# Kernel tuning notes

Measured on AMD Instinct MI355X. Metric: run time of the kernel, lower is better.

## Reference

```python
import jax, jax.numpy as jnp
import numpy as np

B, T, C, H = 4, 2048, 1024, 16
D = C // H
EPS = 1e-5


def setup_inputs() -> dict:
    key = jax.random.key(0)
    ks = jax.random.split(key, 8)
    s = 0.02
    return {
        "hidden_states": jax.random.normal(ks[0], (B, T, C), jnp.float32),
        "w_attn": jax.random.normal(ks[1], (C, 3 * C), jnp.float32) * s,
        "b_attn": jnp.zeros((3 * C,), jnp.float32),
        "w_proj": jax.random.normal(ks[2], (C, C), jnp.float32) * s,
        "b_proj": jnp.zeros((C,), jnp.float32),
        "ln1_g": jnp.ones((C,), jnp.float32),
        "ln1_b": jnp.zeros((C,), jnp.float32),
        "ln2_g": jnp.ones((C,), jnp.float32),
        "ln2_b": jnp.zeros((C,), jnp.float32),
        "w_fc": jax.random.normal(ks[3], (C, 4 * C), jnp.float32) * s,
        "b_fc": jnp.zeros((4 * C,), jnp.float32),
        "w_fc2": jax.random.normal(ks[4], (4 * C, C), jnp.float32) * s,
        "b_fc2": jnp.zeros((C,), jnp.float32),
    }


def _layernorm(x, g, b):
    mu = jnp.mean(x, axis=-1, keepdims=True)
    var = jnp.mean(jnp.square(x - mu), axis=-1, keepdims=True)
    return (x - mu) * jax.lax.rsqrt(var + EPS) * g + b


def _attention(x, w_attn, b_attn, w_proj, b_proj):
    Bx, Tx, Cx = x.shape
    qkv = x @ w_attn + b_attn  # [B,T,3C]  (GCLinear transpose=True => x @ W)
    q, k, v = jnp.split(qkv, 3, axis=-1)
    # [B,T,C] -> [B,H,T,D]
    q = q.reshape(Bx, Tx, H, D).transpose(0, 2, 1, 3)
    k = k.reshape(Bx, Tx, H, D).transpose(0, 2, 1, 3)
    v = v.reshape(Bx, Tx, H, D).transpose(0, 2, 1, 3)
    att = jnp.einsum("bhqd,bhkd->bhqk", q, k) * (1.0 / np.sqrt(D))
    causal = jnp.tril(jnp.ones((Tx, Tx), bool))
    att = jnp.where(causal, att, -jnp.inf)
    att = jax.nn.softmax(att, axis=-1)
    y = jnp.einsum("bhqk,bhkd->bhqd", att, v)
    y = y.transpose(0, 2, 1, 3).reshape(Bx, Tx, Cx)
    return y @ w_proj + b_proj


def reference(hidden_states, w_attn, b_attn, w_proj, b_proj,
              ln1_g, ln1_b, ln2_g, ln2_b, w_fc, b_fc, w_fc2, b_fc2):
    x = hidden_states
    a = _attention(_layernorm(x, ln1_g, ln1_b), w_attn, b_attn, w_proj, b_proj)
    x = x + a
    h = _layernorm(x, ln2_g, ln2_b)
    h = jax.nn.gelu(h @ w_fc + b_fc, approximate=False)  # nn.GELU default = exact erf
    h = h @ w_fc2 + b_fc2
    return x + h
```

## Files before the change

kernel.cpp:

```cpp
#include <hip/hip_runtime.h>
#include <hip/hip_bf16.h>
#include <stdint.h>

typedef __bf16 bf16_t;
typedef __bf16 bf16x8 __attribute__((ext_vector_type(8)));
typedef __bf16 bf16x4 __attribute__((ext_vector_type(4)));
typedef float f32x4 __attribute__((ext_vector_type(4)));
typedef short short4v __attribute__((ext_vector_type(4)));

#define BDIM_B 4
#define TDIM 2048
#define CDIM 1024

__device__ __forceinline__ void gload16(const void* g, void* l) {
  using GP = const __attribute__((address_space(1))) char*;
  using LP = __attribute__((address_space(3))) char*;
  __builtin_amdgcn_global_load_lds((GP)(uintptr_t)g, (LP)(uint32_t)(uintptr_t)l, 16, 0, 0);
}

#define S_BARRIER() asm volatile("s_barrier" ::: "memory")

__global__ __launch_bounds__(256)
void transpose_cast(const float* __restrict__ W, bf16_t* __restrict__ Wt, int K, int N) {
  __shared__ float tile[32][33];
  const int tx = threadIdx.x & 31, ty = threadIdx.x >> 5;
  const int n0 = blockIdx.x * 32, k0 = blockIdx.y * 32;
#pragma unroll
  for (int j = 0; j < 32; j += 8)
    tile[ty + j][tx] = W[(size_t)(k0 + ty + j) * N + n0 + tx];
  __syncthreads();
#pragma unroll
  for (int j = 0; j < 32; j += 8)
    Wt[(size_t)(n0 + ty + j) * K + k0 + tx] = (bf16_t)tile[tx][ty + j];
}

__global__ __launch_bounds__(256)
void transpose_v(const bf16_t* __restrict__ qkv, bf16_t* __restrict__ vT) {
  __shared__ bf16_t tile[64 * 64];
  const int tt = blockIdx.x;
  const int h = blockIdx.y, b = blockIdx.z;
  const int tid = threadIdx.x;
  const int sr = tid >> 3, sc = tid & 7;
  const bf16_t* src = qkv + (size_t)(b * TDIM) * 3072 + 2048 + h * 64;
#pragma unroll
  for (int p = 0; p < 2; ++p) {
    const int t = p * 32 + sr;
    *(uint4*)(tile + t * 64 + ((sc ^ (t & 7)) * 8)) =
        *(const uint4*)(src + (size_t)(tt * 64 + t) * 3072 + sc * 8);
  }
  __syncthreads();
  const int d = tid >> 2, tq = tid & 3;
  bf16_t* dst = vT + ((size_t)((b * 16 + h) * 64 + d)) * TDIM + tt * 64;
#pragma unroll
  for (int p = 0; p < 2; ++p) {
    union { uint4 u; bf16_t e[8]; } o;
#pragma unroll
    for (int j = 0; j < 8; ++j) {
      const int t = p * 32 + tq * 8 + j;
      o.e[j] = tile[t * 64 + (((d >> 3) ^ (t & 7)) * 8) + (d & 7)];
    }
    *(uint4*)(dst + p * 32 + tq * 8) = o.u;
  }
}

__global__ __launch_bounds__(256)
void ln_kernel(const float* __restrict__ x, const float* __restrict__ g,
               const float* __restrict__ bta, bf16_t* __restrict__ out) {
  const size_t row = blockIdx.x;
  const int tid = threadIdx.x;
  const float4 v = ((const float4*)(x + row * CDIM))[tid];
  float s = v.x + v.y + v.z + v.w;
#pragma unroll
  for (int off = 1; off < 64; off <<= 1) s += __shfl_xor(s, off);
  __shared__ float r1[4], r2[4];
  const int wv = tid >> 6, lane = tid & 63;
  if (!lane) r1[wv] = s;
  __syncthreads();
  const float mu = (r1[0] + r1[1] + r1[2] + r1[3]) * (1.f / CDIM);
  const float dx = v.x - mu, dy = v.y - mu, dz = v.z - mu, dw = v.w - mu;
  float q = dx * dx + dy * dy + dz * dz + dw * dw;
#pragma unroll
  for (int off = 1; off < 64; off <<= 1) q += __shfl_xor(q, off);
  if (!lane) r2[wv] = q;
  __syncthreads();
  const float var = (r2[0] + r2[1] + r2[2] + r2[3]) * (1.f / CDIM);
  const float rs = rsqrtf(var + 1e-5f);
  const float4 gg = ((const float4*)g)[tid];
  const float4 bb = ((const float4*)bta)[tid];
  bf16x4 o;
  o[0] = (bf16_t)(dx * rs * gg.x + bb.x);
  o[1] = (bf16_t)(dy * rs * gg.y + bb.y);
  o[2] = (bf16_t)(dz * rs * gg.z + bb.z);
  o[3] = (bf16_t)(dw * rs * gg.w + bb.w);
  ((bf16x4*)(out + row * CDIM))[tid] = o;
}

enum { EPI_BF16 = 0, EPI_RESID = 1, EPI_GELU = 2 };

template <int EPI>
__global__ __launch_bounds__(512)
void gemm256(const bf16_t* __restrict__ A, const bf16_t* __restrict__ Bt,
             const float* __restrict__ bias, const float* __restrict__ resid,
             void* __restrict__ outv, int M, int N, int K) {
  __shared__ bf16_t sA[2][256 * 64];
  __shared__ bf16_t sB[2][256 * 64];
  const int tid = threadIdx.x;
  const int lane = tid & 63, wv = tid >> 6;
  const int wm = wv >> 2, wn = wv & 3;
  const int rin = lane & 15, quad = lane >> 4;

  const int nwg = gridDim.x * gridDim.y;
  const int bid = blockIdx.y * gridDim.x + blockIdx.x;
  const int swzb = (bid & 7) * (nwg >> 3) + (bid >> 3);
  const int bx = swzb % gridDim.x, by = swzb / gridDim.x;
  const int m0 = by * 256, n0 = bx * 256;

  const int r0 = tid >> 3, cc = tid & 7;
  const int sxo = (cc ^ (r0 & 7)) * 8;
  const bf16_t* gA = A + (size_t)(m0 + r0) * K + sxo;
  const bf16_t* gB = Bt + (size_t)(n0 + r0) * K + sxo;
  const int ldst = r0 * 64 + cc * 8;

#define STGA(buf, h, kk) { \
    gload16(gA + (size_t)((h) * 128) * K + (kk), (buf) + (h) * 128 * 64 + ldst);              \
    gload16(gA + (size_t)((h) * 128 + 64) * K + (kk), (buf) + ((h) * 128 + 64) * 64 + ldst); }
#define STGB(buf, h, kk) { \
    gload16(gB + (size_t)((h) * 128) * K + (kk), (buf) + (h) * 128 * 64 + ldst);              \
    gload16(gB + (size_t)((h) * 128 + 64) * K + (kk), (buf) + ((h) * 128 + 64) * 64 + ldst); }

  const int ck0 = (quad ^ (rin & 7)) * 8;
  const int ck1 = ((4 + quad) ^ (rin & 7)) * 8;
  const int aBase = (wm * 128 + rin) * 64;
  const int bBase = (wn * 64 + rin) * 64;

  f32x4 acc[8][4] = {};
  bf16x8 af[8][2], bfr[4][2];

#define RDA(mi) { af[mi][0] = *(const bf16x8*)(rA + aBase + (mi)*1024 + ck0); \
                  af[mi][1] = *(const bf16x8*)(rA + aBase + (mi)*1024 + ck1); }
#define RDB(ni) { bfr[ni][0] = *(const bf16x8*)(rB + bBase + (ni)*1024 + ck0); \
                  bfr[ni][1] = *(const bf16x8*)(rB + bBase + (ni)*1024 + ck1); }
#define MM(mi, ni) { acc[mi][ni] = __builtin_amdgcn_mfma_f32_16x16x32_bf16(af[mi][0], bfr[ni][0], acc[mi][ni], 0, 0, 0); \
                     acc[mi][ni] = __builtin_amdgcn_mfma_f32_16x16x32_bf16(af[mi][1], bfr[ni][1], acc[mi][ni], 0, 0, 0); }

  const int NT = K >> 6;

  {
    const int k1 = (NT > 1 ? 1 : 0) * 64;
    STGA(sA[0], 0, 0); STGB(sB[0], 0, 0); STGA(sA[0], 1, 0); STGB(sB[0], 1, 0);
    STGB(sB[1], 0, k1); STGA(sA[1], 0, k1); STGA(sA[1], 1, k1);
  }
  asm volatile("s_waitcnt vmcnt(6)" ::: "memory");
  S_BARRIER();

  for (int t = 0; t < NT; ++t) {
    const bf16_t* rA = sA[t & 1];
    const bf16_t* rB = sB[t & 1];
    bf16_t* wA = sA[(t & 1) ^ 1];
    bf16_t* wB = sB[(t & 1) ^ 1];
    const int kk1 = (t + 1 < NT ? t + 1 : NT - 1) * 64;
    const int kk2 = (t + 2 < NT ? t + 2 : NT - 1) * 64;

    RDA(0) RDA(1) RDA(2) RDA(3) RDB(0) RDB(1)
    STGB(wB, 1, kk1);
    S_BARRIER();
    __builtin_amdgcn_s_setprio(1);
    MM(0, 0) MM(0, 1) MM(1, 0) MM(1, 1) MM(2, 0) MM(2, 1) MM(3, 0) MM(3, 1)
    __builtin_amdgcn_s_setprio(0);
    S_BARRIER();

    RDB(2) RDB(3)
    S_BARRIER();
    __builtin_amdgcn_s_setprio(1);
    MM(0, 2) MM(0, 3) MM(1, 2) MM(1, 3) MM(2, 2) MM(2, 3) MM(3, 2) MM(3, 3)
    __builtin_amdgcn_s_setprio(0);
    S_BARRIER();

    RDA(4) RDA(5) RDA(6) RDA(7)
    STGB(sB[t & 1], 0, kk2);
    S_BARRIER();
    __builtin_amdgcn_s_setprio(1);
    MM(4, 0) MM(4, 1) MM(5, 0) MM(5, 1) MM(6, 0) MM(6, 1) MM(7, 0) MM(7, 1)
    __builtin_amdgcn_s_setprio(0);
    S_BARRIER();

    STGA(sA[t & 1], 0, kk2); STGA(sA[t & 1], 1, kk2);
    __builtin_amdgcn_s_setprio(1);
    MM(4, 2) MM(4, 3) MM(5, 2) MM(5, 3) MM(6, 2) MM(6, 3) MM(7, 2) MM(7, 3)
    __builtin_amdgcn_s_setprio(0);
    asm volatile("s_waitcnt vmcnt(6)" ::: "memory");
    S_BARRIER();
  }
  asm volatile("s_waitcnt vmcnt(0)" ::: "memory");

  const int rbase = m0 + wm * 128 + quad * 4;
  const int cbase = n0 + wn * 64 + rin;
#pragma unroll
  for (int mi = 0; mi < 8; ++mi)
#pragma unroll
    for (int ni = 0; ni < 4; ++ni)
#pragma unroll
      for (int r = 0; r < 4; ++r) {
        const int m = rbase + mi * 16 + r;
        const int n = cbase + ni * 16;
        float v = acc[mi][ni][r] + bias[n];
        if (EPI == EPI_RESID) v += resid[(size_t)m * N + n];
        if (EPI == EPI_GELU) v = 0.5f * v * (1.0f + erff(v * 0.7071067811865476f));
        if (EPI == EPI_RESID)
          ((float*)outv)[(size_t)m * N + n] = v;
        else
          ((bf16_t*)outv)[(size_t)m * N + n] = (bf16_t)v;
      }
#undef STGA
#undef STGB
#undef RDA
#undef RDB
#undef MM
}

template <int EPI>
__global__ __launch_bounds__(512)
void gemm128(const bf16_t* __restrict__ A, const bf16_t* __restrict__ Bt,
             const float* __restrict__ bias, const float* __restrict__ resid,
             void* __restrict__ outv, int M, int N, int K) {
  __shared__ bf16_t sA[3][256 * 64];
  __shared__ bf16_t sB[3][128 * 64];
  const int tid = threadIdx.x;
  const int lane = tid & 63, wv = tid >> 6;
  const int wm = wv >> 1, wn = wv & 1;
  const int rin = lane & 15, quad = lane >> 4;

  const int nwg = gridDim.x * gridDim.y;
  const int bid = blockIdx.y * gridDim.x + blockIdx.x;
  const int swzb = (bid & 7) * (nwg >> 3) + (bid >> 3);
  const int bx = swzb % gridDim.x, by = swzb / gridDim.x;
  const int m0 = by * 256, n0 = bx * 128;

  const int c8 = (lane & 7) ^ ((lane >> 3) & 7);
  const bf16_t* srcA = A + (size_t)(m0 + 8 * wv + (lane >> 3)) * K + c8 * 8;
  const int dstA = (8 * wv) * 64;
  const bf16_t* srcB = Bt + (size_t)(n0 + (wv >> 2) * 64 + (wv & 3) * 8 + (lane >> 3)) * K + c8 * 8;
  const int dstB = ((wv >> 2) * 64 + (wv & 3) * 8) * 64;

#define STA(buf, r, kk) gload16(srcA + (size_t)(64 * (r)) * K + (kk), (buf) + dstA + 64 * (r) * 64)
#define STB(buf, r, kk) gload16(srcB + (size_t)(32 * (r)) * K + (kk), (buf) + dstB + 32 * (r) * 64)

  const int ck0 = (quad ^ (rin & 7)) * 8;
  const int ck1 = ((4 + quad) ^ (rin & 7)) * 8;
  const int aBase = (wm * 64 + rin) * 64;
  const int bBase = (wn * 64 + rin) * 64;

  f32x4 acc[4][4] = {};
  bf16x8 af[4][2], bfr[4][2];

#define RDA(mi) { af[mi][0] = *(const bf16x8*)(rA + aBase + (mi)*1024 + ck0); \
                  af[mi][1] = *(const bf16x8*)(rA + aBase + (mi)*1024 + ck1); }
#define RDB(ni) { bfr[ni][0] = *(const bf16x8*)(rB + bBase + (ni)*1024 + ck0); \
                  bfr[ni][1] = *(const bf16x8*)(rB + bBase + (ni)*1024 + ck1); }
#define MM(mi, ni) { acc[mi][ni] = __builtin_amdgcn_mfma_f32_16x16x32_bf16(af[mi][0], bfr[ni][0], acc[mi][ni], 0, 0, 0); \
                     acc[mi][ni] = __builtin_amdgcn_mfma_f32_16x16x32_bf16(af[mi][1], bfr[ni][1], acc[mi][ni], 0, 0, 0); }

  const int NT = K >> 6;

  STA(sA[0], 0, 0); STA(sA[0], 1, 0); STA(sA[0], 2, 0); STA(sA[0], 3, 0); STB(sB[0], 0, 0);
  STB(sB[0], 1, 0);
  STA(sA[1], 0, 64); STA(sA[1], 1, 64); STA(sA[1], 2, 64); STA(sA[1], 3, 64); STB(sB[1], 0, 64);
  STB(sB[1], 1, 64);
  asm volatile("s_waitcnt vmcnt(7)" ::: "memory");
  S_BARRIER();

  int rb = 0, wb = 2;
  for (int t = 0; t < NT; ++t) {
    const bf16_t* rA = sA[rb];
    const bf16_t* rB = sB[rb];
    bf16_t* wA = sA[wb];
    bf16_t* wB = sB[wb];
    const int kk = (t + 2 < NT ? t + 2 : NT - 1) * 64;

    RDA(0) RDA(1) RDA(2) RDA(3) RDB(0) RDB(1)
    asm volatile("s_waitcnt vmcnt(6)" ::: "memory");
    S_BARRIER();
    STA(wA, 0, kk); STA(wA, 1, kk); STA(wA, 2, kk); STA(wA, 3, kk); STB(wB, 0, kk);
    __builtin_amdgcn_s_setprio(1);
    MM(0, 0) MM(0, 1) MM(1, 0) MM(1, 1) MM(2, 0) MM(2, 1) MM(3, 0) MM(3, 1)
    __builtin_amdgcn_s_setprio(0);

    RDB(2) RDB(3)
    asm volatile("s_waitcnt vmcnt(6)" ::: "memory");
    S_BARRIER();
    STB(wB, 1, kk);
    __builtin_amdgcn_s_setprio(1);
    MM(0, 2) MM(0, 3) MM(1, 2) MM(1, 3) MM(2, 2) MM(2, 3) MM(3, 2) MM(3, 3)
    __builtin_amdgcn_s_setprio(0);

    rb = (rb == 2) ? 0 : rb + 1;
    wb = (wb == 2) ? 0 : wb + 1;
  }
  asm volatile("s_waitcnt vmcnt(0)" ::: "memory");

  const int rbase = m0 + wm * 64 + quad * 4;
  const int cbase = n0 + wn * 64 + rin;
#pragma unroll
  for (int mi = 0; mi < 4; ++mi)
#pragma unroll
    for (int ni = 0; ni < 4; ++ni)
#pragma unroll
      for (int r = 0; r < 4; ++r) {
        const int m = rbase + mi * 16 + r;
        const int n = cbase + ni * 16;
        float v = acc[mi][ni][r] + bias[n];
        if (EPI == EPI_RESID) v += resid[(size_t)m * N + n];
        if (EPI == EPI_GELU) v = 0.5f * v * (1.0f + erff(v * 0.7071067811865476f));
        if (EPI == EPI_RESID)
          ((float*)outv)[(size_t)m * N + n] = v;
        else
          ((bf16_t*)outv)[(size_t)m * N + n] = (bf16_t)v;
      }
#undef STA
#undef STB
#undef RDA
#undef RDB
#undef MM
}

__global__ __launch_bounds__(256)
void attn_kernel(const bf16_t* __restrict__ qkv, const bf16_t* __restrict__ vT,
                 bf16_t* __restrict__ y) {
  const int id = blockIdx.x;
  const int bx = id >> 6;
  const int h = id & 15, b = (id >> 4) & 3;
  const int tid = threadIdx.x, lane = tid & 63, wv = tid >> 6;
  const int rin = lane & 15, quad = lane >> 4;

  __shared__ bf16_t K2[2][64 * 64];
  __shared__ bf16_t V2[2][64 * 64];

  const size_t base3 = (size_t)(b * TDIM) * 3072;
  const bf16_t* Kg = qkv + base3 + 1024 + h * 64;
  const bf16_t* Vg = vT + (size_t)((b * 16 + h) * 64) * TDIM;
  const int sr = tid >> 3, sc = tid & 7;
  const int sx = (sc ^ (sr & 7)) * 8;
  const short4v ones = {(short)0x3F80, (short)0x3F80, (short)0x3F80, (short)0x3F80};

#define STAGE(bi, kt_) { \
    gload16(Kg + (size_t)((kt_) * 64 + sr) * 3072 + sx,      K2[bi] + sr * 64 + sc * 8);        \
    gload16(Kg + (size_t)((kt_) * 64 + 32 + sr) * 3072 + sx, K2[bi] + (32 + sr) * 64 + sc * 8); \
    gload16(Vg + (size_t)sr * TDIM + (kt_) * 64 + sx,        V2[bi] + sr * 64 + sc * 8);        \
    gload16(Vg + (size_t)(32 + sr) * TDIM + (kt_) * 64 + sx, V2[bi] + (32 + sr) * 64 + sc * 8); }

#pragma unroll 1
  for (int seg = 0; seg < 2; ++seg) {
    const int qt = seg ? bx : (31 - bx);
    const int q0 = qt * 64;
    const int nkt = qt + 1;

    bf16x8 aq[2];
    {
      const size_t qr = base3 + (size_t)(q0 + wv * 16 + rin) * 3072 + h * 64;
      aq[0] = *(const bf16x8*)(qkv + qr + quad * 8);
      aq[1] = *(const bf16x8*)(qkv + qr + 32 + quad * 8);
    }

    f32x4 o[4] = {};
    f32x4 ol = {};

    STAGE(0, 0)
    asm volatile("s_waitcnt vmcnt(0)" ::: "memory");
    S_BARRIER();

    for (int kt = 0; kt < nkt; ++kt) {
      const bf16_t* Kb = K2[kt & 1];
      const bf16_t* Vb = V2[kt & 1];
      if (kt + 1 < nkt) STAGE((kt + 1) & 1, kt + 1)
      f32x4 st[4] = {};
#pragma unroll
      for (int ki = 0; ki < 2; ++ki) {
#pragma unroll
        for (int kf = 0; kf < 4; ++kf) {
          const bf16x8 ak = *(const bf16x8*)(Kb + (kf * 16 + rin) * 64 +
                                             (((ki * 4 + quad) ^ (rin & 7)) * 8));
          st[kf] = __builtin_amdgcn_mfma_f32_16x16x32_bf16(ak, aq[ki], st[kf], 0, 0, 0);
        }
      }
      const bool maskt = (kt == qt);
      const int qg = q0 + wv * 16 + rin;
      short4v pf[4];
#pragma unroll
      for (int kf = 0; kf < 4; ++kf)
#pragma unroll
        for (int r = 0; r < 4; ++r) {
          const int kg = kt * 64 + kf * 16 + quad * 4 + r;
          float p = __builtin_amdgcn_exp2f(st[kf][r] * 0.18033688f);
          if (maskt && kg > qg) p = 0.f;
          union { bf16_t bv; short sv; } cv;
          cv.bv = (bf16_t)p;
          pf[kf][r] = cv.sv;
        }
#pragma unroll
      for (int kf = 0; kf < 4; ++kf) {
#pragma unroll
        for (int nd = 0; nd < 4; ++nd) {
          const short4v bv = *(const short4v*)(Vb + (nd * 16 + rin) * 64 +
                                               (((kf * 2 + (quad >> 1)) ^ (rin & 7)) * 8) +
                                               (quad & 1) * 4);
          o[nd] = __builtin_amdgcn_mfma_f32_16x16x16bf16_1k(pf[kf], bv, o[nd], 0, 0, 0);
        }
        ol = __builtin_amdgcn_mfma_f32_16x16x16bf16_1k(pf[kf], ones, ol, 0, 0, 0);
      }
      asm volatile("s_waitcnt vmcnt(0)" ::: "memory");
      S_BARRIER();
    }

#pragma unroll
    for (int r = 0; r < 4; ++r) {
      const float inv = 1.0f / ol[r];
      const size_t row = (size_t)b * TDIM + q0 + wv * 16 + quad * 4 + r;
#pragma unroll
      for (int nd = 0; nd < 4; ++nd)
        y[row * CDIM + h * 64 + nd * 16 + rin] = (bf16_t)(o[nd][r] * inv);
    }
  }
#undef STAGE
}

extern "C" void kernel_launch(void* const* d_in, const int* in_sizes, int n_in,
                              void* d_out, int out_size, void* d_ws, size_t ws_size,
                              hipStream_t stream) {
  const float* x      = (const float*)d_in[0];
  const float* w_attn = (const float*)d_in[1];
  const float* b_attn = (const float*)d_in[2];
  const float* w_proj = (const float*)d_in[3];
  const float* b_proj = (const float*)d_in[4];
  const float* ln1g   = (const float*)d_in[5];
  const float* ln1b   = (const float*)d_in[6];
  const float* ln2g   = (const float*)d_in[7];
  const float* ln2b   = (const float*)d_in[8];
  const float* w_fc   = (const float*)d_in[9];
  const float* b_fc   = (const float*)d_in[10];
  const float* w_fc2  = (const float*)d_in[11];
  const float* b_fc2  = (const float*)d_in[12];
  float* out = (float*)d_out;

  char* ws = (char*)d_ws;
  bf16_t* wTattn = (bf16_t*)(ws + 0);
  bf16_t* wTproj = (bf16_t*)(ws + 6291456);
  bf16_t* wTfc   = (bf16_t*)(ws + 8388608);
  bf16_t* wTfc2  = (bf16_t*)(ws + 16777216);
  bf16_t* xn     = (bf16_t*)(ws + 25165824);
  float*  x2     = (float*)(ws + 41943040);
  bf16_t* qkv    = (bf16_t*)(ws + 75497472);
  bf16_t* yb     = (bf16_t*)(ws + 75497472 + 50331648);
  bf16_t* hb     = (bf16_t*)(ws + 75497472);
  bf16_t* vT     = xn;

  transpose_cast<<<dim3(96, 32), 256, 0, stream>>>(w_attn, wTattn, 1024, 3072);
  transpose_cast<<<dim3(32, 32), 256, 0, stream>>>(w_proj, wTproj, 1024, 1024);
  transpose_cast<<<dim3(128, 32), 256, 0, stream>>>(w_fc, wTfc, 1024, 4096);
  transpose_cast<<<dim3(32, 128), 256, 0, stream>>>(w_fc2, wTfc2, 4096, 1024);

  ln_kernel<<<8192, 256, 0, stream>>>(x, ln1g, ln1b, xn);
  gemm128<EPI_BF16><<<dim3(24, 32), 512, 0, stream>>>(xn, wTattn, b_attn, nullptr, qkv, 8192, 3072, 1024);
  transpose_v<<<dim3(32, 16, 4), 256, 0, stream>>>(qkv, vT);
  attn_kernel<<<dim3(1024), 256, 0, stream>>>(qkv, vT, yb);
  gemm128<EPI_RESID><<<dim3(8, 32), 512, 0, stream>>>(yb, wTproj, b_proj, x, x2, 8192, 1024, 1024);
  ln_kernel<<<8192, 256, 0, stream>>>(x2, ln2g, ln2b, xn);
  gemm256<EPI_GELU><<<dim3(16, 32), 512, 0, stream>>>(xn, wTfc, b_fc, nullptr, hb, 8192, 4096, 1024);
  gemm128<EPI_RESID><<<dim3(8, 32), 512, 0, stream>>>(hb, wTfc2, b_fc2, x2, out, 8192, 1024, 4096);
}
```

Measured before the change: 482.9 us.

## Simplify GEMM main loops to one barrier per K tile

Both GEMM kernels drop the interleaved multi-phase schedule, where LDS reads, global-to-LDS loads and MFMA groups were split by several barriers per K tile. Each iteration now issues all prefetch loads first, then all LDS fragment reads, then all MFMAs, and ends with one wait and barrier. The large-tile kernel changes from a 2-deep to a 1-deep prefetch with a full vmcnt(0) wait per iteration. The goal is fewer barriers, at the cost of less overlap between global loads and compute and more live fragment registers.

```diff
diff --git a/kernel.cpp b/kernel.cpp
--- a/kernel.cpp
+++ b/kernel.cpp
@@ -145,12 +145,8 @@
 
   const int NT = K >> 6;
 
-  {
-    const int k1 = (NT > 1 ? 1 : 0) * 64;
-    STGA(sA[0], 0, 0); STGB(sB[0], 0, 0); STGA(sA[0], 1, 0); STGB(sB[0], 1, 0);
-    STGB(sB[1], 0, k1); STGA(sA[1], 0, k1); STGA(sA[1], 1, k1);
-  }
-  asm volatile("s_waitcnt vmcnt(6)" ::: "memory");
+  STGA(sA[0], 0, 0); STGA(sA[0], 1, 0); STGB(sB[0], 0, 0); STGB(sB[0], 1, 0);
+  asm volatile("s_waitcnt vmcnt(0)" ::: "memory");
   S_BARRIER();
 
   for (int t = 0; t < NT; ++t) {
@@ -158,40 +154,22 @@
     const bf16_t* rB = sB[t & 1];
     bf16_t* wA = sA[(t & 1) ^ 1];
     bf16_t* wB = sB[(t & 1) ^ 1];
-    const int kk1 = (t + 1 < NT ? t + 1 : NT - 1) * 64;
-    const int kk2 = (t + 2 < NT ? t + 2 : NT - 1) * 64;
-
-    RDA(0) RDA(1) RDA(2) RDA(3) RDB(0) RDB(1)
-    STGB(wB, 1, kk1);
-    S_BARRIER();
+    const int kk = (t + 1 < NT ? t + 1 : t) * 64;
+
+    STGA(wA, 0, kk); STGA(wA, 1, kk); STGB(wB, 0, kk); STGB(wB, 1, kk);
+
+    RDA(0) RDA(1) RDA(2) RDA(3) RDB(0) RDB(1) RDB(2) RDB(3)
+    RDA(4) RDA(5) RDA(6) RDA(7)
     __builtin_amdgcn_s_setprio(1);
     MM(0, 0) MM(0, 1) MM(1, 0) MM(1, 1) MM(2, 0) MM(2, 1) MM(3, 0) MM(3, 1)
-    __builtin_amdgcn_s_setprio(0);
-    S_BARRIER();
-
-    RDB(2) RDB(3)
-    S_BARRIER();
-    __builtin_amdgcn_s_setprio(1);
     MM(0, 2) MM(0, 3) MM(1, 2) MM(1, 3) MM(2, 2) MM(2, 3) MM(3, 2) MM(3, 3)
-    __builtin_amdgcn_s_setprio(0);
-    S_BARRIER();
-
-    RDA(4) RDA(5) RDA(6) RDA(7)
-    STGB(sB[t & 1], 0, kk2);
-    S_BARRIER();
-    __builtin_amdgcn_s_setprio(1);
     MM(4, 0) MM(4, 1) MM(5, 0) MM(5, 1) MM(6, 0) MM(6, 1) MM(7, 0) MM(7, 1)
-    __builtin_amdgcn_s_setprio(0);
-    S_BARRIER();
-
-    STGA(sA[t & 1], 0, kk2); STGA(sA[t & 1], 1, kk2);
-    __builtin_amdgcn_s_setprio(1);
     MM(4, 2) MM(4, 3) MM(5, 2) MM(5, 3) MM(6, 2) MM(6, 3) MM(7, 2) MM(7, 3)
     __builtin_amdgcn_s_setprio(0);
-    asm volatile("s_waitcnt vmcnt(6)" ::: "memory");
+
+    asm volatile("s_waitcnt vmcnt(0)" ::: "memory");
     S_BARRIER();
   }
-  asm volatile("s_waitcnt vmcnt(0)" ::: "memory");
 
   const int rbase = m0 + wm * 128 + quad * 4;
   const int cbase = n0 + wn * 64 + rin;
@@ -262,11 +240,11 @@
 
   const int NT = K >> 6;
 
-  STA(sA[0], 0, 0); STA(sA[0], 1, 0); STA(sA[0], 2, 0); STA(sA[0], 3, 0); STB(sB[0], 0, 0);
-  STB(sB[0], 1, 0);
-  STA(sA[1], 0, 64); STA(sA[1], 1, 64); STA(sA[1], 2, 64); STA(sA[1], 3, 64); STB(sB[1], 0, 64);
-  STB(sB[1], 1, 64);
-  asm volatile("s_waitcnt vmcnt(7)" ::: "memory");
+  STA(sA[0], 0, 0); STA(sA[0], 1, 0); STA(sA[0], 2, 0); STA(sA[0], 3, 0);
+  STB(sB[0], 0, 0); STB(sB[0], 1, 0);
+  STA(sA[1], 0, 64); STA(sA[1], 1, 64); STA(sA[1], 2, 64); STA(sA[1], 3, 64);
+  STB(sB[1], 0, 64); STB(sB[1], 1, 64);
+  asm volatile("s_waitcnt vmcnt(6)" ::: "memory");
   S_BARRIER();
 
   int rb = 0, wb = 2;
@@ -277,21 +255,17 @@
     bf16_t* wB = sB[wb];
     const int kk = (t + 2 < NT ? t + 2 : NT - 1) * 64;
 
-    RDA(0) RDA(1) RDA(2) RDA(3) RDB(0) RDB(1)
+    STA(wA, 0, kk); STA(wA, 1, kk); STA(wA, 2, kk); STA(wA, 3, kk);
+    STB(wB, 0, kk); STB(wB, 1, kk);
+
+    RDA(0) RDA(1) RDA(2) RDA(3) RDB(0) RDB(1) RDB(2) RDB(3)
+    __builtin_amdgcn_s_setprio(1);
+    MM(0, 0) MM(0, 1) MM(1, 0) MM(1, 1) MM(2, 0) MM(2, 1) MM(3, 0) MM(3, 1)
+    MM(0, 2) MM(0, 3) MM(1, 2) MM(1, 3) MM(2, 2) MM(2, 3) MM(3, 2) MM(3, 3)
+    __builtin_amdgcn_s_setprio(0);
+
     asm volatile("s_waitcnt vmcnt(6)" ::: "memory");
     S_BARRIER();
-    STA(wA, 0, kk); STA(wA, 1, kk); STA(wA, 2, kk); STA(wA, 3, kk); STB(wB, 0, kk);
-    __builtin_amdgcn_s_setprio(1);
-    MM(0, 0) MM(0, 1) MM(1, 0) MM(1, 1) MM(2, 0) MM(2, 1) MM(3, 0) MM(3, 1)
-    __builtin_amdgcn_s_setprio(0);
-
-    RDB(2) RDB(3)
-    asm volatile("s_waitcnt vmcnt(6)" ::: "memory");
-    S_BARRIER();
-    STB(wB, 1, kk);
-    __builtin_amdgcn_s_setprio(1);
-    MM(0, 2) MM(0, 3) MM(1, 2) MM(1, 3) MM(2, 2) MM(2, 3) MM(3, 2) MM(3, 3)
-    __builtin_amdgcn_s_setprio(0);
 
     rb = (rb == 2) ? 0 : rb + 1;
     wb = (wb == 2) ? 0 : wb + 1;
```

Measured after the change: 480.6 us. About the same (-0.5%).
